# Kernel optimization log

Measured on AMD Instinct MI355X. Metric: run time of the kernel, lower is better.

## Reference

```python
import jax, jax.numpy as jnp
import numpy as np

B, Cin, Cout, H, W, K = 8, 256, 256, 64, 64, 3  # kernel 3x3, stride 1, pad 1, dilation 1
EPS = 1e-5


def setup_inputs() -> dict:
    key = jax.random.key(0)
    k0, k1, k2 = jax.random.split(key, 3)
    x = jax.random.normal(k0, (B, Cin, H, W), jnp.float32)
    # offset-predicting conv (mmcv zero-inits it; use small random weights so offsets are nontrivial)
    w_off = jax.random.normal(k1, (2 * K * K, Cin, K, K), jnp.float32) * 0.01
    b_off = jnp.zeros((2 * K * K,), jnp.float32)
    # main deformable conv weight
    w = jax.random.normal(k2, (Cout, Cin, K, K), jnp.float32) * (1.0 / np.sqrt(Cin * K * K))
    b = jnp.zeros((Cout,), jnp.float32)
    gamma = jnp.ones((Cout,), jnp.float32)
    beta = jnp.zeros((Cout,), jnp.float32)
    return {"x": x, "w_off": w_off, "b_off": b_off, "w": w, "b": b, "gamma": gamma, "beta": beta}


def _deform_fusion(x, w_off, b_off, w, b, gamma, beta):
    Bn, C, Hh, Ww = x.shape
    # 1) predict offsets: [B, 2*K*K, H, W]; channel layout is (dy, dx) per kernel tap
    offset = jax.lax.conv_general_dilated(x, w_off, (1, 1), ((1, 1), (1, 1)))
    offset = offset + b_off[None, :, None, None]
    off = offset.reshape(Bn, K * K, 2, Hh, Ww)
    dy, dx = off[:, :, 0], off[:, :, 1]  # each [B, K*K, H, W]

    # 2) sampling positions: p = p0 + p_k + delta_p  (stride 1, pad 1 -> p_k in {-1,0,1})
    kk = jnp.arange(K * K)
    ky = (kk // K - (K // 2)).astype(jnp.float32)[None, :, None, None]
    kx = (kk % K - (K // 2)).astype(jnp.float32)[None, :, None, None]
    py = ky + jnp.arange(Hh, dtype=jnp.float32)[None, None, :, None] + dy  # [B,K2,H,W]
    px = kx + jnp.arange(Ww, dtype=jnp.float32)[None, None, None, :] + dx

    # 3) bilinear sampling with zero padding outside the image
    y0 = jnp.floor(py); x0 = jnp.floor(px)
    fy = py - y0; fx = px - x0
    x_flat = x.reshape(Bn, C, Hh * Ww)

    def corner(yi, xi, wgt):
        valid = (yi >= 0) & (yi <= Hh - 1) & (xi >= 0) & (xi <= Ww - 1)
        idx = (jnp.clip(yi, 0, Hh - 1) * Ww + jnp.clip(xi, 0, Ww - 1)).astype(jnp.int32)
        idx = idx.reshape(Bn, -1)  # [B, K2*H*W]
        g = jax.vmap(lambda xf, ii: jnp.take(xf, ii, axis=1))(x_flat, idx)  # [B,C,K2*H*W]
        return g * (wgt * valid).reshape(Bn, 1, -1)

    sampled = (corner(y0,     x0,     (1 - fy) * (1 - fx))
             + corner(y0,     x0 + 1, (1 - fy) * fx)
             + corner(y0 + 1, x0,     fy * (1 - fx))
             + corner(y0 + 1, x0 + 1, fy * fx))  # [B, C, K2*H*W]
    sampled = sampled.reshape(Bn, C, K * K, Hh * Ww)

    # 4) contract sampled patches with conv weight: implicit-GEMM of deformable conv
    out = jnp.einsum('bckp,ock->bop', sampled, w.reshape(w.shape[0], C, K * K))
    out = out + b[None, :, None]
    out = out.reshape(Bn, -1, Hh, Ww)

    # 5) BatchNorm (training-mode batch statistics) + ReLU
    mean = out.mean(axis=(0, 2, 3), keepdims=True)
    var = out.var(axis=(0, 2, 3), keepdims=True)
    out = gamma[None, :, None, None] * (out - mean) * jax.lax.rsqrt(var + EPS) + beta[None, :, None, None]
    return jax.nn.relu(out)


def reference(x, w_off, b_off, w, b, gamma, beta):
    return _deform_fusion(x, w_off, b_off, w, b, gamma, beta)
```

## Files before the change

### kernel.cpp

```cpp
#include <hip/hip_runtime.h>
#include <math.h>

#define BN_ 8
#define CIN 256
#define COUT 256
#define HH 64
#define WW 64
#define HW 4096
#define KK 9
#define OC 18
#define EPS 1e-5f
#define NTOT (BN_ * COUT * HW)

#define OFF_WS 0
#define WTB_WS 589824
#define WOB_WS 884736
#define ST_WS  921600
#define XT_WS  922112

typedef float f32x4 __attribute__((ext_vector_type(4)));
typedef short s16x8 __attribute__((ext_vector_type(8)));

__device__ __forceinline__ unsigned short f2bf(float f) {
  unsigned int u = __float_as_uint(f);
  unsigned int r = (u + 0x7fffu + ((u >> 16) & 1u)) >> 16;
  return (unsigned short)r;
}
__device__ __forceinline__ float bf2f(short s) {
  return __uint_as_float(((unsigned int)(unsigned short)s) << 16);
}

__global__ __launch_bounds__(256) void xpose_kernel(
    const float* __restrict__ x, unsigned short* __restrict__ xt) {
  __shared__ float s[64][65];
  const int t = threadIdx.x;
  const int p0 = blockIdx.x * 64;
  const int c0 = blockIdx.y * 64;
  const int b  = blockIdx.z;
  const float* xb = x + ((size_t)b * CIN + c0) * HW + p0;
#pragma unroll
  for (int pass = 0; pass < 4; ++pass) {
    int cr = pass * 16 + (t >> 4);
    int ps = (t & 15) * 4;
    float4 v = *(const float4*)(xb + (size_t)cr * HW + ps);
    s[ps + 0][cr] = v.x; s[ps + 1][cr] = v.y; s[ps + 2][cr] = v.z; s[ps + 3][cr] = v.w;
  }
  __syncthreads();
  unsigned short* xo = xt + (size_t)b * 32 * HW * 8;
#pragma unroll
  for (int r = 0; r < 2; ++r) {
    int flat = r * 256 + t;
    int pr = flat >> 3, sub = flat & 7;
    int g8 = (c0 >> 3) + sub;
    s16x8 v;
#pragma unroll
    for (int j = 0; j < 8; ++j) v[j] = (short)f2bf(s[pr][sub * 8 + j]);
    *(s16x8*)(xo + ((size_t)g8 * HW + p0 + pr) * 8) = v;
  }
}

__global__ __launch_bounds__(256) void wob_kernel(
    const float* __restrict__ w_off, unsigned short* __restrict__ wob) {
  const int ki = blockIdx.x;
  const int kk = ki >> 3;
  const int cc0 = (ki & 7) << 5;
#pragma unroll
  for (int r = 0; r < 4; ++r) {
    int e = r * 256 + threadIdx.x;
    int g = e >> 8, m = (e >> 3) & 31, j = e & 7;
    int c = cc0 + g * 8 + j;
    unsigned short v = 0;
    if (m < OC) v = f2bf(w_off[((size_t)m * CIN + c) * 9 + kk]);
    wob[(size_t)ki * 1024 + e] = v;
  }
}

__global__ __launch_bounds__(256) void offset_kernel(
    const unsigned short* __restrict__ xt, const unsigned short* __restrict__ wob,
    const float* __restrict__ b_off, float* __restrict__ off_ws) {
  __shared__ __align__(16) char smem[32768];
  const int t = threadIdx.x;
  const int lane = t & 63;
  const int wv = t >> 6;
  const int b = blockIdx.x & 7;
  const int h = blockIdx.x >> 3;
  const unsigned short* xtb = xt + (size_t)b * 32 * HW * 8;
  const int fr = lane & 15, fq = lane >> 4;
  unsigned short* sb = (unsigned short*)smem + wv * 2048;
  float* red = (float*)smem;

  f32x4 acc[2][4] = {};

  for (int s = 0; s < 18; ++s) {
    const int ki = wv * 18 + s;
    const int kk = ki >> 3, cc0 = (ki & 7) << 5;
    const int ky = kk / 3 - 1, kx = kk % 3 - 1;
    const int y = h + ky;
    const bool yok = (y >= 0) && (y < HH);
    const int xcol = lane + kx;
    const bool ok = yok && (xcol >= 0) && (xcol < WW);
    const int pix = y * WW + xcol;

    s16x8 af[2];
    const unsigned short* ap = wob + (size_t)ki * 1024;
#pragma unroll
    for (int i = 0; i < 2; ++i)
      af[i] = *(const s16x8*)&ap[(fq * 32 + i * 16 + fr) * 8];

#pragma unroll
    for (int g = 0; g < 4; ++g) {
      s16x8 v = {0, 0, 0, 0, 0, 0, 0, 0};
      if (ok)
        __builtin_memcpy(&v, (const char*)xtb + ((((size_t)(cc0 >> 3) + g) << 16)) + (size_t)pix * 16, 16);
      *(s16x8*)&sb[(g * 64 + lane) * 8] = v;
    }
    __builtin_amdgcn_s_waitcnt(0);

    s16x8 bf[4];
#pragma unroll
    for (int jn = 0; jn < 4; ++jn)
      bf[jn] = *(const s16x8*)&sb[(fq * 64 + jn * 16 + fr) * 8];
#pragma unroll
    for (int i = 0; i < 2; ++i)
#pragma unroll
      for (int jn = 0; jn < 4; ++jn)
        acc[i][jn] = __builtin_amdgcn_mfma_f32_16x16x32_bf16(af[i], bf[jn], acc[i][jn], 0, 0, 0);
  }

  __syncthreads();
#pragma unroll
  for (int i = 0; i < 2; ++i)
#pragma unroll
    for (int jn = 0; jn < 4; ++jn)
#pragma unroll
      for (int rg = 0; rg < 4; ++rg)
        red[wv * 2048 + (i * 16 + fq * 4 + rg) * 64 + jn * 16 + fr] = acc[i][jn][rg];
  __syncthreads();

  const int m = t >> 3;
  const int pq = (t & 7) * 8;
  float4 v0 = make_float4(0.f, 0.f, 0.f, 0.f), v1 = v0;
#pragma unroll
  for (int w = 0; w < 4; ++w) {
    float4 a = *(float4*)&red[w * 2048 + m * 64 + pq];
    float4 c = *(float4*)&red[w * 2048 + m * 64 + pq + 4];
    v0.x += a.x; v0.y += a.y; v0.z += a.z; v0.w += a.w;
    v1.x += c.x; v1.y += c.y; v1.z += c.z; v1.w += c.w;
  }
  if (m < OC) {
    float bo = b_off[m];
    v0.x += bo; v0.y += bo; v0.z += bo; v0.w += bo;
    v1.x += bo; v1.y += bo; v1.z += bo; v1.w += bo;
    float* op = off_ws + ((size_t)b * OC + m) * HW + h * WW + pq;
    *(float4*)op = v0;
    *(float4*)(op + 4) = v1;
  }
}

__global__ __launch_bounds__(256) void wtrans_kernel(
    const float* __restrict__ w, unsigned short* __restrict__ wTb) {
  const int kb = blockIdx.x;
  const int kk = kb >> 3;
  const int c0 = (kb & 7) << 5;
  const int o = threadIdx.x;
#pragma unroll
  for (int g = 0; g < 4; ++g)
#pragma unroll
    for (int j = 0; j < 8; ++j) {
      int c = c0 + g * 8 + j;
      wTb[(((size_t)kb * 4 + g) * 256 + o) * 8 + j] =
          f2bf(w[((size_t)o * CIN + c) * 9 + kk]);
    }
}

__global__ __launch_bounds__(512, 4) void gemm_kernel(
    const unsigned short* __restrict__ xt, const unsigned short* __restrict__ wTb,
    const float* __restrict__ off_ws, const float* __restrict__ bias,
    float* __restrict__ out, float* __restrict__ stats) {
  __shared__ unsigned short s_b[2][4096];
  const int t = threadIdx.x;
  const int lane = t & 63;
  const int wv = t >> 6;
  const int b = blockIdx.x & 7;
  const int h = blockIdx.x >> 3;
  const int p0 = h * 64;
  const int col = t & 63;
  const int oct = t >> 6;
  const int fr = lane & 15, fq = lane >> 4;
  const unsigned short* xtb = xt + (size_t)b * 32 * HW * 8;
  const float* offp = off_ws + (size_t)b * OC * HW + p0 + col;

  int cofs[4];
  float qw[4], qwN[4];

  auto calc = [&](int kk, float dy, float dx) {
    float py = (float)(kk / 3 - 1 + h) + dy;
    float pxx = (float)(kk % 3 - 1 + col) + dx;
    float y0f = floorf(py), x0f = floorf(pxx);
    float fy = py - y0f, fx = pxx - x0f;
    int y0 = (int)y0f, x0 = (int)x0f;
    int y1 = y0 + 1, x1 = x0 + 1;
    bool vy0 = (y0 >= 0) && (y0 < HH), vy1 = (y1 >= 0) && (y1 < HH);
    bool vx0 = (x0 >= 0) && (x0 < WW), vx1 = (x1 >= 0) && (x1 < WW);
    int cy0 = min(max(y0, 0), HH - 1), cy1 = min(max(y1, 0), HH - 1);
    int cx0 = min(max(x0, 0), WW - 1), cx1 = min(max(x1, 0), WW - 1);
    cofs[0] = (cy0 * WW + cx0) * 16;  qwN[0] = (vy0 && vx0) ? (1.f - fy) * (1.f - fx) : 0.f;
    cofs[1] = (cy0 * WW + cx1) * 16;  qwN[1] = (vy0 && vx1) ? (1.f - fy) * fx : 0.f;
    cofs[2] = (cy1 * WW + cx0) * 16;  qwN[2] = (vy1 && vx0) ? fy * (1.f - fx) : 0.f;
    cofs[3] = (cy1 * WW + cx1) * 16;  qwN[3] = (vy1 && vx1) ? fy * fx : 0.f;
  };

  s16x8 gE[4], gO[4];

  auto gather = [&](int chunk64, s16x8* g) {
    const char* bp = (const char*)xtb + (((size_t)(chunk64 * 8 + oct)) << 16);
#pragma unroll
    for (int k = 0; k < 4; ++k)
      __builtin_memcpy(&g[k], bp + cofs[k], 16);
  };

  auto combine_write = [&](int buf, const s16x8* g) {
    s16x8 v;
#pragma unroll
    for (int j = 0; j < 8; ++j) {
      float val = 0.f;
#pragma unroll
      for (int k = 0; k < 4; ++k)
        val = fmaf(qw[k], bf2f(g[k][j]), val);
      v[j] = (short)f2bf(val);
    }
    *(s16x8*)&s_b[buf][(oct * 64 + col) * 8] = v;
  };

  auto load_a = [&](int iter, s16x8 af[2][2]) {
#pragma unroll
    for (int ks = 0; ks < 2; ++ks) {
      const unsigned short* ap =
          wTb + (((size_t)(iter * 2 + ks) * 4 + fq) * 256 + wv * 32 + fr) * 8;
#pragma unroll
      for (int i = 0; i < 2; ++i)
        af[ks][i] = *(const s16x8*)(ap + (size_t)i * 16 * 8);
    }
  };

  f32x4 acc[2][4] = {};
  float dyp, dxp;

  {
    float dy0 = offp[0];
    float dx0 = offp[HW];
    calc(0, dy0, dx0);
#pragma unroll
    for (int k2 = 0; k2 < 4; ++k2) qw[k2] = qwN[k2];
    dyp = offp[2 * HW];
    dxp = offp[3 * HW];
    gather(0, gE);
    gather(1, gO);
    combine_write(0, gE);
  }
  asm volatile("s_waitcnt lgkmcnt(0)" ::: "memory");
  __builtin_amdgcn_s_barrier();

#define GBODY(I, GW, GR, CUR)                                                  \
  {                                                                            \
    s16x8 af[2][2];                                                            \
    load_a(I, af);                                                             \
    const int nx1 = (I) + 1, nx2 = (I) + 2;                                    \
    bool newq = false;                                                         \
    if (nx1 < 36) {                                                            \
      if (nx2 < 36) {                                                          \
        if ((nx2 & 3) == 0) {                                                  \
          const int kkc = nx2 >> 2;                                            \
          calc(kkc, dyp, dxp);                                                 \
          newq = true;                                                         \
          const int kkn = kkc + 1;                                             \
          if (kkn < 9) {                                                       \
            dyp = offp[(size_t)(2 * kkn) * HW];                                \
            dxp = offp[(size_t)(2 * kkn + 1) * HW];                            \
          }                                                                    \
        }                                                                      \
        gather((nx2) & 3, GW);                                                 \
      }                                                                        \
      combine_write((CUR) ^ 1, GR);                                            \
      if (newq) {                                                              \
        _Pragma("unroll")                                                      \
        for (int k2 = 0; k2 < 4; ++k2) qw[k2] = qwN[k2];                       \
      }                                                                        \
    }                                                                          \
    _Pragma("unroll")                                                          \
    for (int ks = 0; ks < 2; ++ks)                                             \
      _Pragma("unroll")                                                        \
      for (int jj = 0; jj < 4; ++jj) {                                         \
        s16x8 bfr = *(const s16x8*)&s_b[CUR][((ks * 4 + fq) * 64 + jj * 16 + fr) * 8]; \
        _Pragma("unroll")                                                      \
        for (int ii = 0; ii < 2; ++ii)                                         \
          acc[ii][jj] = __builtin_amdgcn_mfma_f32_16x16x32_bf16(               \
              af[ks][ii], bfr, acc[ii][jj], 0, 0, 0);                          \
      }                                                                        \
    asm volatile("s_waitcnt lgkmcnt(0)" ::: "memory");                         \
    __builtin_amdgcn_s_barrier();                                              \
  }

  for (int m = 0; m < 18; ++m) {
    const int i0 = 2 * m;
    GBODY(i0, gE, gO, 0)
    GBODY(i0 + 1, gO, gE, 1)
  }
#undef GBODY

#pragma unroll
  for (int i = 0; i < 2; ++i) {
#pragma unroll
    for (int rg = 0; rg < 4; ++rg) {
      int o = wv * 32 + i * 16 + fq * 4 + rg;
      float bv = bias[o];
      float* op = out + ((size_t)(b * COUT + o)) * HW + p0 + fr;
      float s = 0.f, s2 = 0.f;
#pragma unroll
      for (int j = 0; j < 4; ++j) {
        float val = acc[i][j][rg] + bv;
        op[j * 16] = val;
        s += val; s2 += val * val;
      }
#pragma unroll
      for (int m2 = 1; m2 < 16; m2 <<= 1) {
        s += __shfl_xor(s, m2);
        s2 += __shfl_xor(s2, m2);
      }
      if (fr == 0) {
        atomicAdd(&stats[o], s);
        atomicAdd(&stats[COUT + o], s2);
      }
    }
  }
}

__global__ __launch_bounds__(256) void bn_kernel(
    float* __restrict__ out, const float* __restrict__ stats,
    const float* __restrict__ gamma, const float* __restrict__ beta) {
  int i4 = (blockIdx.x * 256 + threadIdx.x) * 4;
  int o = (i4 >> 12) & (COUT - 1);
  const float inv_n = 1.f / (float)(BN_ * HW);
  float mean = stats[o] * inv_n;
  float var = stats[COUT + o] * inv_n - mean * mean;
  float sc = gamma[o] * rsqrtf(var + EPS);
  float sh = beta[o] - mean * sc;
  float4 v = *(float4*)(out + i4);
  v.x = fmaxf(fmaf(v.x, sc, sh), 0.f);
  v.y = fmaxf(fmaf(v.y, sc, sh), 0.f);
  v.z = fmaxf(fmaf(v.z, sc, sh), 0.f);
  v.w = fmaxf(fmaf(v.w, sc, sh), 0.f);
  *(float4*)(out + i4) = v;
}

extern "C" void kernel_launch(void* const* d_in, const int* in_sizes, int n_in,
                              void* d_out, int out_size, void* d_ws, size_t ws_size,
                              hipStream_t stream) {
  const float* x     = (const float*)d_in[0];
  const float* w_off = (const float*)d_in[1];
  const float* b_off = (const float*)d_in[2];
  const float* w     = (const float*)d_in[3];
  const float* bias  = (const float*)d_in[4];
  const float* gamma = (const float*)d_in[5];
  const float* beta  = (const float*)d_in[6];
  float* out = (float*)d_out;
  float* ws = (float*)d_ws;
  float* off_ws = ws + OFF_WS;
  unsigned short* wTb = (unsigned short*)(ws + WTB_WS);
  unsigned short* wob = (unsigned short*)(ws + WOB_WS);
  float* stats = ws + ST_WS;
  unsigned short* xt = (unsigned short*)(ws + XT_WS);

  hipMemsetAsync(stats, 0, 2 * COUT * sizeof(float), stream);
  xpose_kernel<<<dim3(64, 4, 8), 256, 0, stream>>>(x, xt);
  wob_kernel<<<72, 256, 0, stream>>>(w_off, wob);
  wtrans_kernel<<<72, 256, 0, stream>>>(w, wTb);
  offset_kernel<<<512, 256, 0, stream>>>(xt, wob, b_off, off_ws);
  gemm_kernel<<<512, 512, 0, stream>>>(xt, wTb, off_ws, bias, out, stats);
  bn_kernel<<<NTOT / 1024, 256, 0, stream>>>(out, stats, gamma, beta);
}
```

Before: 229.8 us.

## Restructure gemm pipeline, pack bf16 combine, merge prep kernels and memset

Merges the two weight-reformatting kernels and the stats memset into one prep kernel, which saves launches. Inside the deformable GEMM, the pipeline changes from a two-deep gather with double register sets to a single gather buffer. The next A fragments are prefetched into registers, and the bilinear combine plus shared write moves after the MFMA block, with s_setprio raised around the MFMAs. The combine uses packed f32x2 FMAs and v_cvt_pk_bf16_f32 (round-to-nearest-even, so the result matches the previous rounding). This lowers register pressure and VALU work, but global gather latency now has less slack to hide behind.

New measurement: 221.3 us. -3.7%, faster.

```diff
diff --git a/kernel.cpp b/kernel.cpp
--- a/kernel.cpp
+++ b/kernel.cpp
@@ -19,7 +19,9 @@
 #define XT_WS  922112
 
 typedef float f32x4 __attribute__((ext_vector_type(4)));
+typedef float f32x2 __attribute__((ext_vector_type(2)));
 typedef short s16x8 __attribute__((ext_vector_type(8)));
+typedef unsigned int u32x4 __attribute__((ext_vector_type(4)));
 
 __device__ __forceinline__ unsigned short f2bf(float f) {
   unsigned int u = __float_as_uint(f);
@@ -59,20 +61,32 @@
   }
 }
 
-__global__ __launch_bounds__(256) void wob_kernel(
-    const float* __restrict__ w_off, unsigned short* __restrict__ wob) {
-  const int ki = blockIdx.x;
-  const int kk = ki >> 3;
-  const int cc0 = (ki & 7) << 5;
+__global__ __launch_bounds__(256) void prep_kernel(
+    const float* __restrict__ w_off, const float* __restrict__ w,
+    unsigned short* __restrict__ wob, unsigned short* __restrict__ wTb,
+    float* __restrict__ stats) {
+  const int kb = blockIdx.x;
+  const int kk = kb >> 3;
+  const int c0 = (kb & 7) << 5;
+  const int t = threadIdx.x;
+  if (kb == 71) { stats[t] = 0.f; stats[256 + t] = 0.f; }
 #pragma unroll
   for (int r = 0; r < 4; ++r) {
-    int e = r * 256 + threadIdx.x;
+    int e = r * 256 + t;
     int g = e >> 8, m = (e >> 3) & 31, j = e & 7;
-    int c = cc0 + g * 8 + j;
+    int c = c0 + g * 8 + j;
     unsigned short v = 0;
     if (m < OC) v = f2bf(w_off[((size_t)m * CIN + c) * 9 + kk]);
-    wob[(size_t)ki * 1024 + e] = v;
-  }
+    wob[(size_t)kb * 1024 + e] = v;
+  }
+#pragma unroll
+  for (int g = 0; g < 4; ++g)
+#pragma unroll
+    for (int j = 0; j < 8; ++j) {
+      int c = c0 + g * 8 + j;
+      wTb[(((size_t)kb * 4 + g) * 256 + t) * 8 + j] =
+          f2bf(w[((size_t)t * CIN + c) * 9 + kk]);
+    }
 }
 
 __global__ __launch_bounds__(256) void offset_kernel(
@@ -155,22 +169,6 @@
     *(float4*)op = v0;
     *(float4*)(op + 4) = v1;
   }
-}
-
-__global__ __launch_bounds__(256) void wtrans_kernel(
-    const float* __restrict__ w, unsigned short* __restrict__ wTb) {
-  const int kb = blockIdx.x;
-  const int kk = kb >> 3;
-  const int c0 = (kb & 7) << 5;
-  const int o = threadIdx.x;
-#pragma unroll
-  for (int g = 0; g < 4; ++g)
-#pragma unroll
-    for (int j = 0; j < 8; ++j) {
-      int c = c0 + g * 8 + j;
-      wTb[(((size_t)kb * 4 + g) * 256 + o) * 8 + j] =
-          f2bf(w[((size_t)o * CIN + c) * 9 + kk]);
-    }
 }
 
 __global__ __launch_bounds__(512, 4) void gemm_kernel(
@@ -191,7 +189,7 @@
   const float* offp = off_ws + (size_t)b * OC * HW + p0 + col;
 
   int cofs[4];
-  float qw[4], qwN[4];
+  f32x2 qw2[4];
 
   auto calc = [&](int kk, float dy, float dx) {
     float py = (float)(kk / 3 - 1 + h) + dy;
@@ -204,32 +202,43 @@
     bool vx0 = (x0 >= 0) && (x0 < WW), vx1 = (x1 >= 0) && (x1 < WW);
     int cy0 = min(max(y0, 0), HH - 1), cy1 = min(max(y1, 0), HH - 1);
     int cx0 = min(max(x0, 0), WW - 1), cx1 = min(max(x1, 0), WW - 1);
-    cofs[0] = (cy0 * WW + cx0) * 16;  qwN[0] = (vy0 && vx0) ? (1.f - fy) * (1.f - fx) : 0.f;
-    cofs[1] = (cy0 * WW + cx1) * 16;  qwN[1] = (vy0 && vx1) ? (1.f - fy) * fx : 0.f;
-    cofs[2] = (cy1 * WW + cx0) * 16;  qwN[2] = (vy1 && vx0) ? fy * (1.f - fx) : 0.f;
-    cofs[3] = (cy1 * WW + cx1) * 16;  qwN[3] = (vy1 && vx1) ? fy * fx : 0.f;
+    float q0 = (vy0 && vx0) ? (1.f - fy) * (1.f - fx) : 0.f;
+    float q1 = (vy0 && vx1) ? (1.f - fy) * fx : 0.f;
+    float q2 = (vy1 && vx0) ? fy * (1.f - fx) : 0.f;
+    float q3 = (vy1 && vx1) ? fy * fx : 0.f;
+    cofs[0] = (cy0 * WW + cx0) * 16;  qw2[0][0] = q0; qw2[0][1] = q0;
+    cofs[1] = (cy0 * WW + cx1) * 16;  qw2[1][0] = q1; qw2[1][1] = q1;
+    cofs[2] = (cy1 * WW + cx0) * 16;  qw2[2][0] = q2; qw2[2][1] = q2;
+    cofs[3] = (cy1 * WW + cx1) * 16;  qw2[3][0] = q3; qw2[3][1] = q3;
   };
 
-  s16x8 gE[4], gO[4];
-
-  auto gather = [&](int chunk64, s16x8* g) {
+  s16x8 g[4];
+
+  auto gather = [&](int chunk64) {
     const char* bp = (const char*)xtb + (((size_t)(chunk64 * 8 + oct)) << 16);
 #pragma unroll
     for (int k = 0; k < 4; ++k)
       __builtin_memcpy(&g[k], bp + cofs[k], 16);
   };
 
-  auto combine_write = [&](int buf, const s16x8* g) {
-    s16x8 v;
-#pragma unroll
-    for (int j = 0; j < 8; ++j) {
-      float val = 0.f;
-#pragma unroll
-      for (int k = 0; k < 4; ++k)
-        val = fmaf(qw[k], bf2f(g[k][j]), val);
-      v[j] = (short)f2bf(val);
-    }
-    *(s16x8*)&s_b[buf][(oct * 64 + col) * 8] = v;
+  auto combine_write = [&](int buf) {
+    u32x4 vout;
+#pragma unroll
+    for (int jp = 0; jp < 4; ++jp) {
+      f32x2 a = {0.f, 0.f};
+#pragma unroll
+      for (int k = 0; k < 4; ++k) {
+        unsigned int pr = ((const unsigned int*)&g[k])[jp];
+        f32x2 xv;
+        xv[0] = __uint_as_float(pr << 16);
+        xv[1] = __uint_as_float(pr & 0xffff0000u);
+        a = __builtin_elementwise_fma(qw2[k], xv, a);
+      }
+      unsigned int packed;
+      asm("v_cvt_pk_bf16_f32 %0, %1, %2" : "=v"(packed) : "v"(a[0]), "v"(a[1]));
+      vout[jp] = packed;
+    }
+    *(u32x4*)&s_b[buf][(oct * 64 + col) * 8] = vout;
   };
 
   auto load_a = [&](int iter, s16x8 af[2][2]) {
@@ -244,49 +253,39 @@
   };
 
   f32x4 acc[2][4] = {};
+  s16x8 afE[2][2], afO[2][2];
   float dyp, dxp;
 
   {
     float dy0 = offp[0];
     float dx0 = offp[HW];
     calc(0, dy0, dx0);
-#pragma unroll
-    for (int k2 = 0; k2 < 4; ++k2) qw[k2] = qwN[k2];
     dyp = offp[2 * HW];
     dxp = offp[3 * HW];
-    gather(0, gE);
-    gather(1, gO);
-    combine_write(0, gE);
+    gather(0);
+    load_a(0, afE);
+    combine_write(0);
   }
   asm volatile("s_waitcnt lgkmcnt(0)" ::: "memory");
   __builtin_amdgcn_s_barrier();
 
-#define GBODY(I, GW, GR, CUR)                                                  \
+#define GBODY(I, AFC, AFN, CUR)                                                \
   {                                                                            \
-    s16x8 af[2][2];                                                            \
-    load_a(I, af);                                                             \
-    const int nx1 = (I) + 1, nx2 = (I) + 2;                                    \
-    bool newq = false;                                                         \
+    const int nx1 = (I) + 1;                                                   \
     if (nx1 < 36) {                                                            \
-      if (nx2 < 36) {                                                          \
-        if ((nx2 & 3) == 0) {                                                  \
-          const int kkc = nx2 >> 2;                                            \
-          calc(kkc, dyp, dxp);                                                 \
-          newq = true;                                                         \
-          const int kkn = kkc + 1;                                             \
-          if (kkn < 9) {                                                       \
-            dyp = offp[(size_t)(2 * kkn) * HW];                                \
-            dxp = offp[(size_t)(2 * kkn + 1) * HW];                            \
-          }                                                                    \
+      if ((nx1 & 3) == 0) {                                                    \
+        const int kkc = nx1 >> 2;                                              \
+        calc(kkc, dyp, dxp);                                                   \
+        const int kkn = kkc + 1;                                               \
+        if (kkn < 9) {                                                         \
+          dyp = offp[(size_t)(2 * kkn) * HW];                                  \
+          dxp = offp[(size_t)(2 * kkn + 1) * HW];                              \
         }                                                                      \
-        gather((nx2) & 3, GW);                                                 \
       }                                                                        \
-      combine_write((CUR) ^ 1, GR);                                            \
-      if (newq) {                                                              \
-        _Pragma("unroll")                                                      \
-        for (int k2 = 0; k2 < 4; ++k2) qw[k2] = qwN[k2];                       \
-      }                                                                        \
+      gather(nx1 & 3);                                                         \
+      load_a(nx1, AFN);                                                        \
     }                                                                          \
+    __builtin_amdgcn_s_setprio(1);                                             \
     _Pragma("unroll")                                                          \
     for (int ks = 0; ks < 2; ++ks)                                             \
       _Pragma("unroll")                                                        \
@@ -295,16 +294,20 @@
         _Pragma("unroll")                                                      \
         for (int ii = 0; ii < 2; ++ii)                                         \
           acc[ii][jj] = __builtin_amdgcn_mfma_f32_16x16x32_bf16(               \
-              af[ks][ii], bfr, acc[ii][jj], 0, 0, 0);                          \
+              AFC[ks][ii], bfr, acc[ii][jj], 0, 0, 0);                         \
       }                                                                        \
-    asm volatile("s_waitcnt lgkmcnt(0)" ::: "memory");                         \
-    __builtin_amdgcn_s_barrier();                                              \
+    __builtin_amdgcn_s_setprio(0);                                             \
+    if (nx1 < 36) {                                                            \
+      combine_write((CUR) ^ 1);                                                \
+      asm volatile("s_waitcnt lgkmcnt(0)" ::: "memory");                       \
+      __builtin_amdgcn_s_barrier();                                            \
+    }                                                                          \
   }
 
   for (int m = 0; m < 18; ++m) {
     const int i0 = 2 * m;
-    GBODY(i0, gE, gO, 0)
-    GBODY(i0 + 1, gO, gE, 1)
+    GBODY(i0, afE, afO, 0)
+    GBODY(i0 + 1, afO, afE, 1)
   }
 #undef GBODY
 
@@ -371,10 +374,8 @@
   float* stats = ws + ST_WS;
   unsigned short* xt = (unsigned short*)(ws + XT_WS);
 
-  hipMemsetAsync(stats, 0, 2 * COUT * sizeof(float), stream);
   xpose_kernel<<<dim3(64, 4, 8), 256, 0, stream>>>(x, xt);
-  wob_kernel<<<72, 256, 0, stream>>>(w_off, wob);
-  wtrans_kernel<<<72, 256, 0, stream>>>(w, wTb);
+  prep_kernel<<<72, 256, 0, stream>>>(w_off, w, wob, wTb, stats);
   offset_kernel<<<512, 256, 0, stream>>>(xt, wob, b_off, off_ws);
   gemm_kernel<<<512, 512, 0, stream>>>(xt, wTb, off_ws, bias, out, stats);
   bn_kernel<<<NTOT / 1024, 256, 0, stream>>>(out, stats, gamma, beta);
```
